# Optimization experiments

Measured on AMD Instinct MI355X. Metric: run time of the kernel, lower is better.

The kernel has to match this reference:

```python
import math
import jax, jax.numpy as jnp
import numpy as np

T, D, H = 2048, 2048, 16
C = D // H
EPS = 1e-6


def _rope_tables(c, t):
    inv_freq = 1.0 / (10000.0 ** (jnp.arange(0, c, 2, dtype=jnp.float32) / c))
    freqs = jnp.arange(t, dtype=jnp.float32)[:, None] * inv_freq[None, :]  # (T, C/2)
    return jnp.sin(freqs), jnp.cos(freqs)


def _rotate_every_two(x):
    x1 = x[..., ::2]
    x2 = x[..., 1::2]
    return jnp.stack((-x2, x1), axis=-1).reshape(x.shape)


def _apply_rope(x_htc, sin, cos):
    # sin/cos: (T, C/2) -> repeat each freq twice along channel -> (1, T, C)
    sin = jnp.repeat(sin, 2, axis=-1)[None]
    cos = jnp.repeat(cos, 2, axis=-1)[None]
    return x_htc * cos + _rotate_every_two(x_htc) * sin


def _layernorm(x, w):
    mu = jnp.mean(x, axis=-1, keepdims=True)
    var = jnp.var(x, axis=-1, keepdims=True)
    return (x - mu) / jnp.sqrt(var + EPS) * w


def setup_inputs() -> dict:
    key = jax.random.key(0)
    ks = jax.random.split(key, 4)
    x = jax.random.normal(ks[0], (T, D), dtype=jnp.float32)
    W_attn = jax.random.normal(ks[1], (3 * D, D), dtype=jnp.float32) * 0.02
    b_attn = jnp.zeros((3 * D,), dtype=jnp.float32)
    W_proj = jax.random.normal(ks[2], (D, D), dtype=jnp.float32) * 0.02
    b_proj = jnp.zeros((D,), dtype=jnp.float32)
    q_ln_w = jnp.ones((C,), dtype=jnp.float32)
    k_ln_w = jnp.ones((C,), dtype=jnp.float32)
    return {"x": x, "W_attn": W_attn, "b_attn": b_attn, "W_proj": W_proj,
            "b_proj": b_proj, "q_ln_w": q_ln_w, "k_ln_w": k_ln_w}


def reference(x, W_attn, b_attn, W_proj, b_proj, q_ln_w, k_ln_w):
    t, d = x.shape
    qkv = x @ W_attn.T + b_attn                      # (T, 3D)
    q, k, v = jnp.split(qkv, 3, axis=-1)
    q = q.reshape(t, H, C).transpose(1, 0, 2)        # (H, T, C)
    k = k.reshape(t, H, C).transpose(1, 0, 2)
    v = v.reshape(t, H, C).transpose(1, 0, 2)
    q = _layernorm(q, q_ln_w)
    k = _layernorm(k, k_ln_w)
    sin, cos = _rope_tables(C, t)
    q = _apply_rope(q, sin, cos)
    k = _apply_rope(k, sin, cos)
    a = jnp.einsum("htc,hsc->hts", q, k)             # (H, T, T)
    causal = jnp.tril(jnp.ones((1, t, t))) == 0
    a = jnp.where(causal, float("-inf"), a)
    scaling = math.sqrt(C)                            # q_ln active
    a = jax.nn.softmax(a.astype(jnp.float32) / scaling, axis=-1).astype(x.dtype)
    out = jnp.einsum("hts,hsc->htc", a, v)           # (H, T, C)
    out = out.transpose(1, 0, 2).reshape(t, d)       # (T, D)
    return out @ W_proj.T + b_proj
```

## Files before the change

### kernel.cpp

```cpp
#include <hip/hip_runtime.h>
#include <hip/hip_bf16.h>
#include <math.h>

#define T_DIM 2048
#define D_DIM 2048
#define H_DIM 16
#define C_DIM 128

typedef __bf16 bf16;
typedef __attribute__((ext_vector_type(8))) __bf16 bf16x8;
typedef __attribute__((ext_vector_type(4))) __bf16 bf16x4;
typedef __attribute__((ext_vector_type(2))) __bf16 bf16x2;
typedef __attribute__((ext_vector_type(4))) float f32x4;

__device__ __forceinline__ void gload_lds16(const void* g, void* l) {
  __builtin_amdgcn_global_load_lds((__attribute__((address_space(1))) void*)g,
                                   (__attribute__((address_space(3))) void*)l,
                                   16, 0, 0);
}

__global__ __launch_bounds__(256) void cvt3(
    const float* __restrict__ x, const float* __restrict__ wa, const float* __restrict__ wp,
    bf16* __restrict__ xo, bf16* __restrict__ wao, bf16* __restrict__ wpo)
{
  const int NX = 1048576, NA = 3145728;
  int i = blockIdx.x * 256 + threadIdx.x;
  for (; i < 5242880; i += 2048 * 256) {
    const float* s; bf16* d; int off;
    if (i < NX)            { s = x;  d = xo;  off = i; }
    else if (i < NX + NA)  { s = wa; d = wao; off = i - NX; }
    else                   { s = wp; d = wpo; off = i - NX - NA; }
    float4 v = reinterpret_cast<const float4*>(s)[off];
    bf16x4 o;
    o[0] = (bf16)v.x; o[1] = (bf16)v.y; o[2] = (bf16)v.z; o[3] = (bf16)v.w;
    reinterpret_cast<bf16x4*>(d)[off] = o;
  }
}

template <typename OutT>
__global__ __launch_bounds__(512, 2) void gemm384_bt_bias(
    const bf16* __restrict__ A, const bf16* __restrict__ B,
    const float* __restrict__ bias, OutT* __restrict__ C,
    int M, int N, int K)
{
  __shared__ __align__(16) bf16 Asl[2][128 * 64];
  __shared__ __align__(16) bf16 Bsl[2][384 * 64];
  const int tid = threadIdx.x;
  const int lane = tid & 63;
  const int wv = tid >> 6;
  const int g = lane >> 4, r16 = lane & 15;
  const int wm = wv >> 2;
  const int wn = wv & 3;

  int bid = blockIdx.x;
  int bid2 = (bid & 7) * (gridDim.x >> 3) + (bid >> 3);
  const int ntn = N / 384;
  const int bn = bid2 % ntn, bm = bid2 / ntn;

  const size_t Abase = (size_t)(bm * 128) * K;
  const size_t Bbase = (size_t)(bn * 384) * K;

  f32x4 acc[2][2][2][3] = {};
  bf16x8 a0[2][2], a1[2][2];
  bf16x8 b0[3][2], b1[3][2];

  auto stageA = [&](int bb, int t) {
#pragma unroll
    for (int i = 0; i < 2; ++i) {
      int c = i * 512 + tid;
      int r = c >> 3, p = c & 7, j = p ^ (r & 7);
      gload_lds16(A + Abase + (size_t)r * K + t * 64 + j * 8,
                  (char*)&Asl[bb][0] + (size_t)c * 16);
    }
  };
  auto stageB = [&](int bb, int u, int t) {
#pragma unroll
    for (int i = 0; i < 2; ++i) {
      int c = i * 512 + tid;
      int r = c >> 3, p = c & 7, j = p ^ (r & 7);
      gload_lds16(B + Bbase + (size_t)(u * 128 + r) * K + t * 64 + j * 8,
                  (char*)&Bsl[bb][0] + u * 16384 + (size_t)c * 16);
    }
  };
  auto readAh = [&](bf16x8 (&dst)[2][2], int bufi, int qr) {
#pragma unroll
    for (int R = 0; R < 2; ++R) {
      int ar = wm * 64 + qr * 32 + R * 16 + r16;
#pragma unroll
      for (int ks = 0; ks < 2; ++ks)
        dst[R][ks] = *reinterpret_cast<const bf16x8*>(
            &Asl[bufi][ar * 64 + (((ks * 4 + g) ^ (ar & 7)) << 3)]);
    }
  };
  auto readBh = [&](bf16x8 (&dst)[3][2], int bufi, int qc) {
#pragma unroll
    for (int F = 0; F < 3; ++F) {
      int br = wn * 96 + qc * 48 + F * 16 + r16;
#pragma unroll
      for (int ks = 0; ks < 2; ++ks)
        dst[F][ks] = *reinterpret_cast<const bf16x8*>(
            &Bsl[bufi][br * 64 + (((ks * 4 + g) ^ (br & 7)) << 3)]);
    }
  };
  auto mfma12 = [&](f32x4 (&cq)[2][3], bf16x8 (&aa)[2][2], bf16x8 (&bb)[3][2]) {
#pragma unroll
    for (int ks = 0; ks < 2; ++ks)
#pragma unroll
      for (int R = 0; R < 2; ++R)
#pragma unroll
        for (int F = 0; F < 3; ++F)
          cq[R][F] = __builtin_amdgcn_mfma_f32_16x16x32_bf16(aa[R][ks], bb[F][ks], cq[R][F], 0, 0, 0);
  };

  stageA(0, 0); stageB(0, 0, 0); stageB(0, 1, 0); stageB(0, 2, 0);
  __syncthreads();

  const int NT = K >> 6;
  for (int t = 0; t < NT; ++t) {
    const int cb = t & 1, nb = cb ^ 1;
    if (t + 1 < NT) {
      stageA(nb, t + 1); stageB(nb, 0, t + 1); stageB(nb, 1, t + 1); stageB(nb, 2, t + 1);
    }
    readAh(a0, cb, 0); readAh(a1, cb, 1);
    readBh(b0, cb, 0); readBh(b1, cb, 1);
    mfma12(acc[0][0], a0, b0);
    mfma12(acc[0][1], a0, b1);
    mfma12(acc[1][1], a1, b1);
    mfma12(acc[1][0], a1, b0);
    __syncthreads();
  }

#pragma unroll
  for (int qr = 0; qr < 2; ++qr)
#pragma unroll
    for (int qc = 0; qc < 2; ++qc)
#pragma unroll
      for (int R = 0; R < 2; ++R)
#pragma unroll
        for (int F = 0; F < 3; ++F) {
          int row0 = bm * 128 + wm * 64 + qr * 32 + R * 16 + g * 4;
          int col  = bn * 384 + wn * 96 + qc * 48 + F * 16 + r16;
          float bv = bias[col];
#pragma unroll
          for (int rr = 0; rr < 4; ++rr)
            C[(size_t)(row0 + rr) * N + col] = (OutT)(acc[qr][qc][R][F][rr] + bv);
        }
}

__global__ __launch_bounds__(256, 2) void gemm_bt_bias(
    const bf16* __restrict__ A, const bf16* __restrict__ B,
    const float* __restrict__ bias, float* __restrict__ C,
    int M, int N, int K)
{
  __shared__ __align__(16) bf16 As[2][128 * 64];
  __shared__ __align__(16) bf16 Bs[2][128 * 64];
  const int tid = threadIdx.x;
  const int lane = tid & 63;
  const int w = tid >> 6;
  const int wm = (w >> 1) * 64, wn = (w & 1) * 64;
  const int g = lane >> 4;
  const int r16 = lane & 15;

  int lb = blockIdx.y * gridDim.x + blockIdx.x;
  int nblk = gridDim.x * gridDim.y;
  int s = (lb & 7) * (nblk >> 3) + (lb >> 3);
  const int bn = s % gridDim.x, bm = s / gridDim.x;

  f32x4 acc[4][4] = {};

  const size_t Abase = (size_t)(bm * 128) * K;
  const size_t Bbase = (size_t)(bn * 128) * K;

  auto stage = [&](int bb, int t) {
#pragma unroll
    for (int i = 0; i < 4; ++i) {
      int c = i * 256 + tid;
      int r = c >> 3, p = c & 7, j = p ^ (r & 7);
      gload_lds16(A + Abase + (size_t)r * K + t * 64 + j * 8,
                  (char*)&As[bb][0] + (size_t)c * 16);
      gload_lds16(B + Bbase + (size_t)r * K + t * 64 + j * 8,
                  (char*)&Bs[bb][0] + (size_t)c * 16);
    }
  };

  stage(0, 0);
  __syncthreads();

  const int NT = K >> 6;
  for (int t = 0; t < NT; ++t) {
    const int cb = t & 1, nb = cb ^ 1;
    if (t + 1 < NT) stage(nb, t + 1);
    bf16x8 a[4][2], b[4][2];
#pragma unroll
    for (int m = 0; m < 4; ++m) {
      int ar = wm + m * 16 + r16;
#pragma unroll
      for (int ks = 0; ks < 2; ++ks)
        a[m][ks] = *reinterpret_cast<const bf16x8*>(
            &As[cb][ar * 64 + (((ks * 4 + g) ^ (ar & 7)) << 3)]);
    }
#pragma unroll
    for (int n = 0; n < 4; ++n) {
      int br = wn + n * 16 + r16;
#pragma unroll
      for (int ks = 0; ks < 2; ++ks)
        b[n][ks] = *reinterpret_cast<const bf16x8*>(
            &Bs[cb][br * 64 + (((ks * 4 + g) ^ (br & 7)) << 3)]);
    }
#pragma unroll
    for (int ks = 0; ks < 2; ++ks)
#pragma unroll
      for (int m = 0; m < 4; ++m)
#pragma unroll
        for (int n = 0; n < 4; ++n)
          acc[m][n] = __builtin_amdgcn_mfma_f32_16x16x32_bf16(a[m][ks], b[n][ks], acc[m][n], 0, 0, 0);
    __syncthreads();
  }

#pragma unroll
  for (int m = 0; m < 4; ++m) {
    int row0 = bm * 128 + wm + m * 16 + g * 4;
#pragma unroll
    for (int n = 0; n < 4; ++n) {
      int col = bn * 128 + wn + n * 16 + r16;
      float bv = bias[col];
#pragma unroll
      for (int rr = 0; rr < 4; ++rr)
        C[(size_t)(row0 + rr) * N + col] = acc[m][n][rr] + bv;
    }
  }
}

__global__ __launch_bounds__(256) void lnrope_vt_kernel(
    const bf16* __restrict__ qkv, const float* __restrict__ qw,
    const float* __restrict__ kw, bf16* __restrict__ qo, bf16* __restrict__ ko,
    bf16* __restrict__ vt)
{
  __shared__ bf16 tile[32][33];
  const int tid = threadIdx.x;
  if (blockIdx.x < 8192) {
    const int lane = tid & 63;
    const int wid = blockIdx.x * 4 + (tid >> 6);
    const int h = wid >> 11;
    const int t = wid & (T_DIM - 1);
    const int c0 = lane * 2;

    float inv_freq = exp2f(-13.287712379549449f * (float)c0 * (1.0f / 128.0f));
    float fr = (float)t * inv_freq;
    float sn = sinf(fr), cs = cosf(fr);
    const float scaleq = 0.08838834764831845f;

#pragma unroll
    for (int which = 0; which < 2; ++which) {
      const bf16* base = qkv + (size_t)t * (3 * D_DIM) + which * D_DIM + h * C_DIM;
      bf16x2 v2 = *reinterpret_cast<const bf16x2*>(base + c0);
      float vx = (float)v2[0], vy = (float)v2[1];
      float s = vx + vy;
#pragma unroll
      for (int m = 32; m; m >>= 1) s += __shfl_xor(s, m);
      float mu = s * (1.0f / 128.0f);
      float d0 = vx - mu, d1 = vy - mu;
      float ss = d0 * d0 + d1 * d1;
#pragma unroll
      for (int m = 32; m; m >>= 1) ss += __shfl_xor(ss, m);
      float rstd = rsqrtf(ss * (1.0f / 128.0f) + 1e-6f);
      const float* wgt = which ? kw : qw;
      float x0 = d0 * rstd * wgt[c0], x1 = d1 * rstd * wgt[c0 + 1];
      float o0 = x0 * cs - x1 * sn;
      float o1 = x1 * cs + x0 * sn;
      if (!which) { o0 *= scaleq; o1 *= scaleq; }
      bf16* out = (which ? ko : qo) + ((size_t)h * T_DIM + t) * C_DIM + c0;
      bf16x2 ob; ob[0] = (bf16)o0; ob[1] = (bf16)o1;
      *reinterpret_cast<bf16x2*>(out) = ob;
    }
  } else {
    const int vb = blockIdx.x - 8192;
    const int t0 = (vb & 63) * 32;
    const int c0 = ((vb >> 6) & 3) * 32;
    const int h = vb >> 8;
    const int tx = tid & 31, ty = tid >> 5;
#pragma unroll
    for (int i = 0; i < 4; ++i) {
      int t = t0 + ty + i * 8;
      tile[ty + i * 8][tx] =
          qkv[(size_t)t * (3 * D_DIM) + 2 * D_DIM + h * C_DIM + c0 + tx];
    }
    __syncthreads();
#pragma unroll
    for (int i = 0; i < 4; ++i) {
      int c = c0 + ty + i * 8;
      vt[((size_t)h * C_DIM + c) * T_DIM + t0 + tx] = tile[tx][ty + i * 8];
    }
  }
}

__global__ __launch_bounds__(256, 4) void attn_kernel(
    const bf16* __restrict__ Q, const bf16* __restrict__ K,
    const bf16* __restrict__ VT, bf16* __restrict__ AO,
    float* __restrict__ U, float* __restrict__ ML)
{
  __shared__ __align__(16) bf16 Ks[2][32 * 128];
  __shared__ __align__(16) bf16 Vs[2][128 * 32];
  __shared__ __align__(16) bf16 p_lds[4][16 * 32];
  const int tid = threadIdx.x;
  const int lane = tid & 63;
  const int w = tid >> 6;
  const int g = lane >> 4, r16 = lane & 15;
  const int h = blockIdx.y;
  const int b = blockIdx.x;

  int qb, kb0, kb1, sp;
  if (b < 32) { qb = 16 + (b >> 1); sp = b & 1; kb0 = sp * 32; kb1 = sp ? (2 * qb + 2) : 32; }
  else        { qb = 47 - b;        sp = -1;    kb0 = 0;       kb1 = 2 * qb + 2; }
  const int qr0 = qb * 64 + w * 16;
  const int qrow = qr0 + r16;

  const bf16* Qh = Q + (size_t)h * T_DIM * C_DIM;
  const bf16* Kh = K + (size_t)h * T_DIM * C_DIM;
  const bf16* Vh = VT + (size_t)h * C_DIM * T_DIM;

  bf16x8 qf[4];
#pragma unroll
  for (int kk = 0; kk < 4; ++kk)
    qf[kk] = *reinterpret_cast<const bf16x8*>(
        &Qh[(size_t)qrow * C_DIM + kk * 32 + g * 8]);

  float mrow = -INFINITY, lrow = 0.f;
  f32x4 o[8] = {};

  auto stage = [&](int bb, int kb) {
    const bf16* Kt = Kh + (size_t)(kb * 32) * C_DIM;
    const bf16* Vt = Vh + kb * 32;
#pragma unroll
    for (int i = 0; i < 2; ++i) {
      int e = i * 256 + tid;
      int r = e >> 4, p = e & 15, j = p ^ (r & 7);
      gload_lds16(Kt + r * C_DIM + j * 8, (char*)&Ks[bb][0] + (size_t)e * 16);
    }
#pragma unroll
    for (int i = 0; i < 2; ++i) {
      int e = i * 256 + tid;
      int r = e >> 2, p = e & 3, j = p ^ ((r >> 1) & 3);
      gload_lds16(Vt + (size_t)r * T_DIM + j * 8, (char*)&Vs[bb][0] + (size_t)e * 16);
    }
  };

  stage(0, kb0);
  __syncthreads();
  int buf = 0;

  for (int kb = kb0; kb < kb1; ++kb) {
    if (kb + 1 < kb1) stage(buf ^ 1, kb + 1);

    f32x4 sacc[2] = {};
    __builtin_amdgcn_s_setprio(1);
#pragma unroll
    for (int n = 0; n < 2; ++n) {
      int kr = n * 16 + r16;
      const bf16* kbase = &Ks[buf][kr << 7];
#pragma unroll
      for (int kk = 0; kk < 4; ++kk) {
        bf16x8 kf = *reinterpret_cast<const bf16x8*>(
            kbase + (((kk * 4 + g) ^ (kr & 7)) << 3));
        sacc[n] = __builtin_amdgcn_mfma_f32_16x16x32_bf16(kf, qf[kk], sacc[n], 0, 0, 0);
      }
    }
    __builtin_amdgcn_s_setprio(0);
    if (kb * 32 + 31 > qr0) {
#pragma unroll
      for (int n = 0; n < 2; ++n)
#pragma unroll
        for (int rr = 0; rr < 4; ++rr)
          if (kb * 32 + n * 16 + g * 4 + rr > qrow) sacc[n][rr] = -3.0e38f;
    }
    float mx = fmaxf(fmaxf(fmaxf(sacc[0][0], sacc[0][1]), fmaxf(sacc[0][2], sacc[0][3])),
                     fmaxf(fmaxf(sacc[1][0], sacc[1][1]), fmaxf(sacc[1][2], sacc[1][3])));
    mx = fmaxf(mx, __shfl_xor(mx, 16));
    mx = fmaxf(mx, __shfl_xor(mx, 32));
    float alpha = 1.0f;
    bool need = __any(mx > mrow + 8.0f);
    if (need) {
      float mnew = fmaxf(mrow, mx);
      alpha = __expf(mrow - mnew);
      mrow = mnew;
    }
    float ps = 0.f;
#pragma unroll
    for (int n = 0; n < 2; ++n)
#pragma unroll
      for (int rr = 0; rr < 4; ++rr) {
        float p = __expf(sacc[n][rr] - mrow);
        sacc[n][rr] = p;
        ps += p;
      }
    ps += __shfl_xor(ps, 16);
    ps += __shfl_xor(ps, 32);
    lrow = lrow * alpha + ps;
    if (need) {
#pragma unroll
      for (int nc = 0; nc < 8; ++nc)
#pragma unroll
        for (int rr = 0; rr < 4; ++rr)
          o[nc][rr] *= alpha;
    }
    {
      bf16* prow = &p_lds[w][r16 << 5];
      const int ssw = (r16 >> 1) & 3;
#pragma unroll
      for (int n = 0; n < 2; ++n) {
        bf16x4 pk;
        pk[0] = (bf16)sacc[n][0]; pk[1] = (bf16)sacc[n][1];
        pk[2] = (bf16)sacc[n][2]; pk[3] = (bf16)sacc[n][3];
        int c8 = 2 * n + (g >> 1);
        *reinterpret_cast<bf16x4*>(prow + (((c8 ^ ssw) << 3) | ((g & 1) << 2))) = pk;
      }
    }
    asm volatile("s_waitcnt lgkmcnt(0)" ::: "memory");
    __builtin_amdgcn_s_setprio(1);
    bf16x8 pf = *reinterpret_cast<const bf16x8*>(
        &p_lds[w][(r16 << 5) + ((g ^ ((r16 >> 1) & 3)) << 3)]);
#pragma unroll
    for (int nc = 0; nc < 8; ++nc) {
      int vr = nc * 16 + r16;
      bf16x8 vf = *reinterpret_cast<const bf16x8*>(
          &Vs[buf][(vr << 5) + ((g ^ ((vr >> 1) & 3)) << 3)]);
      o[nc] = __builtin_amdgcn_mfma_f32_16x16x32_bf16(vf, pf, o[nc], 0, 0, 0);
    }
    __builtin_amdgcn_s_setprio(0);
    __syncthreads();
    buf ^= 1;
  }

  if (sp < 0) {
    float inv = 1.0f / lrow;
    bf16* arow = &AO[(size_t)qrow * D_DIM + h * C_DIM + (g << 2)];
#pragma unroll
    for (int nc = 0; nc < 8; ++nc) {
      bf16x4 ob;
      ob[0] = (bf16)(o[nc][0] * inv); ob[1] = (bf16)(o[nc][1] * inv);
      ob[2] = (bf16)(o[nc][2] * inv); ob[3] = (bf16)(o[nc][3] * inv);
      *reinterpret_cast<bf16x4*>(arow + nc * 16) = ob;
    }
  } else {
    const int qi = qb - 16;
    const size_t ubase = ((size_t)(h * 16 + qi) * 2 + sp) * (64 * 128);
    const size_t mlbase = (size_t)(h * 16 + qi) * 256 + sp * 128;
    const int row = w * 16 + r16;
    float* urow = &U[ubase + (size_t)row * 128 + (g << 2)];
#pragma unroll
    for (int nc = 0; nc < 8; ++nc)
      *reinterpret_cast<f32x4*>(urow + nc * 16) = o[nc];
    if (g == 0) {
      ML[mlbase + row] = mrow;
      ML[mlbase + 64 + row] = lrow;
    }
  }
}

__global__ __launch_bounds__(256) void attn_combine(
    const float* __restrict__ U, const float* __restrict__ ML, bf16* __restrict__ AO)
{
  int idx = blockIdx.x * 256 + threadIdx.x;
  int c4 = (idx & 31) * 4;
  int r = idx >> 5;
  int trow = r & 63;
  int qi = (r >> 6) & 15;
  int h = r >> 10;

  size_t mlbase = (size_t)(h * 16 + qi) * 256;
  float m0 = ML[mlbase + trow],       l0 = ML[mlbase + 64 + trow];
  float m1 = ML[mlbase + 128 + trow], l1 = ML[mlbase + 192 + trow];
  float m = fmaxf(m0, m1);
  float a0 = __expf(m0 - m), a1 = __expf(m1 - m);
  float inv = 1.0f / (l0 * a0 + l1 * a1);

  size_t t0 = ((size_t)(h * 16 + qi) * 2) * (64 * 128) + (size_t)trow * 128 + c4;
  float4 u0 = *reinterpret_cast<const float4*>(U + t0);
  float4 u1 = *reinterpret_cast<const float4*>(U + t0 + 64 * 128);
  int t = 1024 + qi * 64 + trow;
  bf16x4 ob;
  ob[0] = (bf16)((u0.x * a0 + u1.x * a1) * inv);
  ob[1] = (bf16)((u0.y * a0 + u1.y * a1) * inv);
  ob[2] = (bf16)((u0.z * a0 + u1.z * a1) * inv);
  ob[3] = (bf16)((u0.w * a0 + u1.w * a1) * inv);
  *reinterpret_cast<bf16x4*>(&AO[(size_t)t * D_DIM + h * C_DIM + c4]) = ob;
}

extern "C" void kernel_launch(void* const* d_in, const int* in_sizes, int n_in,
                              void* d_out, int out_size, void* d_ws, size_t ws_size,
                              hipStream_t stream)
{
  const float* x      = (const float*)d_in[0];
  const float* W_attn = (const float*)d_in[1];
  const float* b_attn = (const float*)d_in[2];
  const float* W_proj = (const float*)d_in[3];
  const float* b_proj = (const float*)d_in[4];
  const float* q_ln_w = (const float*)d_in[5];
  const float* k_ln_w = (const float*)d_in[6];

  char* ws = (char*)d_ws;
  bf16*  x_bf  = (bf16*)(ws + 0);
  bf16*  wa_bf = (bf16*)(ws + 8388608);
  bf16*  wp_bf = (bf16*)(ws + 33554432);
  bf16*  qkv   = (bf16*)(ws + 41943040);
  float* U     = (float*)(ws + 67108864);
  float* ML    = (float*)(ws + 83886080);
  bf16*  q_bf  = (bf16*)(ws + 92274688);
  bf16*  k_bf  = (bf16*)(ws + 100663296);
  bf16*  vt    = (bf16*)(ws + 109051904);
  bf16*  ao    = (bf16*)(ws + 117440512);

  cvt3<<<2048, 256, 0, stream>>>(x, W_attn, W_proj, x_bf, wa_bf, wp_bf);

  gemm384_bt_bias<bf16><<<dim3((T_DIM / 128) * (3 * D_DIM / 384)), dim3(512), 0, stream>>>(
      x_bf, wa_bf, b_attn, qkv, T_DIM, 3 * D_DIM, D_DIM);

  lnrope_vt_kernel<<<8192 + 4096, 256, 0, stream>>>(qkv, q_ln_w, k_ln_w, q_bf, k_bf, vt);

  attn_kernel<<<dim3(48, H_DIM), 256, 0, stream>>>(q_bf, k_bf, vt, ao, U, ML);
  attn_combine<<<2048, 256, 0, stream>>>(U, ML, ao);

  gemm_bt_bias<<<dim3(D_DIM / 128, T_DIM / 128), 256, 0, stream>>>(
      ao, wp_bf, b_proj, (float*)d_out, T_DIM, D_DIM, D_DIM);
}
```

Measured before the change: 170.3 us.

## Rebalance causal attention split-KV: 2-way for mid blocks, 3-way for late

Changes how causal query blocks are split across KV ranges. The first 8 query blocks run unsplit, the middle 16 are split into two halves, and the last 8 into three segments, giving 64 blocks per head instead of 48. The goal is to even out per-block work and raise occupancy during the long attention phase. The combine kernel now merges a variable 2 or 3 partial results over more rows, and the U/ML scratch buffers are moved to reuse the x_bf/wa_bf workspace region. This adds more partial-output traffic and combine work.

```diff
diff --git a/kernel.cpp b/kernel.cpp
--- a/kernel.cpp
+++ b/kernel.cpp
@@ -310,8 +310,17 @@
   const int b = blockIdx.x;
 
   int qb, kb0, kb1, sp;
-  if (b < 32) { qb = 16 + (b >> 1); sp = b & 1; kb0 = sp * 32; kb1 = sp ? (2 * qb + 2) : 32; }
-  else        { qb = 47 - b;        sp = -1;    kb0 = 0;       kb1 = 2 * qb + 2; }
+  if (b < 8) {
+    qb = b; sp = -1; kb0 = 0; kb1 = 2 * b + 2;
+  } else if (b < 40) {
+    int j = b - 8; qb = 8 + (j >> 1); sp = j & 1;
+    int hl = (2 * qb + 2) >> 1;
+    kb0 = sp * hl; kb1 = kb0 + hl;
+  } else {
+    int j = b - 40; int q3 = j / 3; qb = 24 + q3; sp = j - q3 * 3;
+    int n = 2 * qb + 2;
+    kb0 = (n * sp) / 3; kb1 = (n * (sp + 1)) / 3;
+  }
   const int qr0 = qb * 64 + w * 16;
   const int qrow = qr0 + r16;
 
@@ -442,17 +451,18 @@
       *reinterpret_cast<bf16x4*>(arow + nc * 16) = ob;
     }
   } else {
-    const int qi = qb - 16;
-    const size_t ubase = ((size_t)(h * 16 + qi) * 2 + sp) * (64 * 128);
-    const size_t mlbase = (size_t)(h * 16 + qi) * 256 + sp * 128;
+    const int qi = qb - 8;
+    const int slot = (h * 24 + qi) * 3 + sp;
+    const size_t ubase = (size_t)slot * (64 * 128);
+    const size_t mlb = (size_t)slot * 128;
     const int row = w * 16 + r16;
     float* urow = &U[ubase + (size_t)row * 128 + (g << 2)];
 #pragma unroll
     for (int nc = 0; nc < 8; ++nc)
       *reinterpret_cast<f32x4*>(urow + nc * 16) = o[nc];
     if (g == 0) {
-      ML[mlbase + row] = mrow;
-      ML[mlbase + 64 + row] = lrow;
+      ML[mlb + row] = mrow;
+      ML[mlb + 64 + row] = lrow;
     }
   }
 }
@@ -464,25 +474,29 @@
   int c4 = (idx & 31) * 4;
   int r = idx >> 5;
   int trow = r & 63;
-  int qi = (r >> 6) & 15;
-  int h = r >> 10;
-
-  size_t mlbase = (size_t)(h * 16 + qi) * 256;
-  float m0 = ML[mlbase + trow],       l0 = ML[mlbase + 64 + trow];
-  float m1 = ML[mlbase + 128 + trow], l1 = ML[mlbase + 192 + trow];
-  float m = fmaxf(m0, m1);
-  float a0 = __expf(m0 - m), a1 = __expf(m1 - m);
-  float inv = 1.0f / (l0 * a0 + l1 * a1);
-
-  size_t t0 = ((size_t)(h * 16 + qi) * 2) * (64 * 128) + (size_t)trow * 128 + c4;
-  float4 u0 = *reinterpret_cast<const float4*>(U + t0);
-  float4 u1 = *reinterpret_cast<const float4*>(U + t0 + 64 * 128);
-  int t = 1024 + qi * 64 + trow;
+  int hq = r >> 6;
+  int qi = hq % 24;
+  int h = hq / 24;
+  const int nseg = (qi < 16) ? 2 : 3;
+
+  size_t mlb = (size_t)hq * 3 * 128;
+  float m = -INFINITY;
+  for (int s = 0; s < nseg; ++s)
+    m = fmaxf(m, ML[mlb + s * 128 + trow]);
+  float L = 0.f;
+  float ox = 0.f, oy = 0.f, oz = 0.f, ow = 0.f;
+  for (int s = 0; s < nseg; ++s) {
+    float a = __expf(ML[mlb + s * 128 + trow] - m);
+    L += ML[mlb + s * 128 + 64 + trow] * a;
+    float4 u = *reinterpret_cast<const float4*>(
+        U + (size_t)(hq * 3 + s) * (64 * 128) + (size_t)trow * 128 + c4);
+    ox += u.x * a; oy += u.y * a; oz += u.z * a; ow += u.w * a;
+  }
+  float inv = 1.0f / L;
+  int t = (qi + 8) * 64 + trow;
   bf16x4 ob;
-  ob[0] = (bf16)((u0.x * a0 + u1.x * a1) * inv);
-  ob[1] = (bf16)((u0.y * a0 + u1.y * a1) * inv);
-  ob[2] = (bf16)((u0.z * a0 + u1.z * a1) * inv);
-  ob[3] = (bf16)((u0.w * a0 + u1.w * a1) * inv);
+  ob[0] = (bf16)(ox * inv); ob[1] = (bf16)(oy * inv);
+  ob[2] = (bf16)(oz * inv); ob[3] = (bf16)(ow * inv);
   *reinterpret_cast<bf16x4*>(&AO[(size_t)t * D_DIM + h * C_DIM + c4]) = ob;
 }
 
@@ -501,14 +515,14 @@
   char* ws = (char*)d_ws;
   bf16*  x_bf  = (bf16*)(ws + 0);
   bf16*  wa_bf = (bf16*)(ws + 8388608);
-  bf16*  wp_bf = (bf16*)(ws + 33554432);
   bf16*  qkv   = (bf16*)(ws + 41943040);
-  float* U     = (float*)(ws + 67108864);
-  float* ML    = (float*)(ws + 83886080);
-  bf16*  q_bf  = (bf16*)(ws + 92274688);
-  bf16*  k_bf  = (bf16*)(ws + 100663296);
-  bf16*  vt    = (bf16*)(ws + 109051904);
-  bf16*  ao    = (bf16*)(ws + 117440512);
+  bf16*  q_bf  = (bf16*)(ws + 67108864);
+  bf16*  k_bf  = (bf16*)(ws + 75497472);
+  bf16*  vt    = (bf16*)(ws + 83886080);
+  bf16*  ao    = (bf16*)(ws + 92274688);
+  bf16*  wp_bf = (bf16*)(ws + 100663296);
+  float* U  = (float*)(ws + 0);
+  float* ML = (float*)(ws + 37748736);
 
   cvt3<<<2048, 256, 0, stream>>>(x, W_attn, W_proj, x_bf, wa_bf, wp_bf);
 
@@ -517,8 +531,8 @@
 
   lnrope_vt_kernel<<<8192 + 4096, 256, 0, stream>>>(qkv, q_ln_w, k_ln_w, q_bf, k_bf, vt);
 
-  attn_kernel<<<dim3(48, H_DIM), 256, 0, stream>>>(q_bf, k_bf, vt, ao, U, ML);
-  attn_combine<<<2048, 256, 0, stream>>>(U, ML, ao);
+  attn_kernel<<<dim3(64, H_DIM), 256, 0, stream>>>(q_bf, k_bf, vt, ao, U, ML);
+  attn_combine<<<3072, 256, 0, stream>>>(U, ML, ao);
 
   gemm_bt_bias<<<dim3(D_DIM / 128, T_DIM / 128), 256, 0, stream>>>(
       ao, wp_bf, b_proj, (float*)d_out, T_DIM, D_DIM, D_DIM);
```

New measurement: 173.8 us. 1.02x slower.
